# Kernel optimization log

Measured on AMD Instinct MI355X. Metric: run time of the kernel, lower is better.

Reference implementation:

```python
import jax, jax.numpy as jnp
import numpy as np

L, V, C, H, T_MAX, FF = 8, 50257, 1024, 16, 1024, 4096
DH = C // H
EPS = 1e-5


def setup_inputs() -> dict:
    key = jax.random.key(0)
    ks = jax.random.split(key, 16)
    s = 0.02
    inp = {
        "idx": jax.random.randint(ks[0], (2, 1024), 0, V, dtype=jnp.int32),
        "tok_emb": jax.random.normal(ks[1], (V, C), jnp.float32) * s,
        "pos_emb": jax.random.normal(ks[2], (T_MAX, C), jnp.float32) * s,
        "qkv_w": jax.random.normal(ks[3], (L, C, 3 * C), jnp.float32) * s,
        "qkv_b": jnp.zeros((L, 3 * C), jnp.float32),
        "out_w": jax.random.normal(ks[4], (L, C, C), jnp.float32) * s,
        "out_b": jnp.zeros((L, C), jnp.float32),
        "ln1_s": jnp.ones((L, C), jnp.float32),
        "ln1_b": jnp.zeros((L, C), jnp.float32),
        "ln2_s": jnp.ones((L, C), jnp.float32),
        "ln2_b": jnp.zeros((L, C), jnp.float32),
        "ffn_w1": jax.random.normal(ks[5], (L, C, FF), jnp.float32) * s,
        "ffn_b1": jnp.zeros((L, FF), jnp.float32),
        "ffn_w2": jax.random.normal(ks[6], (L, FF, C), jnp.float32) * s,
        "ffn_b2": jnp.zeros((L, C), jnp.float32),
        "lnf_s": jnp.ones((C,), jnp.float32),
        "lnf_b": jnp.zeros((C,), jnp.float32),
    }
    return inp


def _layernorm(x, scale, bias):
    m = jnp.mean(x, axis=-1, keepdims=True)
    v = jnp.mean(jnp.square(x - m), axis=-1, keepdims=True)
    return (x - m) * jax.lax.rsqrt(v + EPS) * scale + bias


def reference(idx, tok_emb, pos_emb, qkv_w, qkv_b, out_w, out_b,
              ln1_s, ln1_b, ln2_s, ln2_b,
              ffn_w1, ffn_b1, ffn_w2, ffn_b2, lnf_s, lnf_b):
    B, T = idx.shape
    x = tok_emb[idx] + pos_emb[:T]          # [B,T,C]
    causal = jnp.tril(jnp.ones((T, T), bool))  # [T,T]
    scale = 1.0 / np.sqrt(DH)

    def block(x, p):
        qw, qb, ow, ob, l1s, l1b, l2s, l2b, w1, b1, w2, b2 = p
        h = _layernorm(x, l1s, l1b)
        qkv = h @ qw + qb                    # [B,T,3C]
        q, k, v = jnp.split(qkv, 3, axis=-1)
        q = q.reshape(B, T, H, DH).transpose(0, 2, 1, 3)  # [B,H,T,Dh]
        k = k.reshape(B, T, H, DH).transpose(0, 2, 1, 3)
        v = v.reshape(B, T, H, DH).transpose(0, 2, 1, 3)
        scores = jnp.einsum('bhqd,bhkd->bhqk', q, k) * scale
        scores = jnp.where(causal, scores, -jnp.inf)
        w = jax.nn.softmax(scores, axis=-1)
        o = jnp.einsum('bhqk,bhkd->bhqd', w, v)
        o = o.transpose(0, 2, 1, 3).reshape(B, T, C)
        x = x + (o @ ow + ob)
        h2 = _layernorm(x, l2s, l2b)
        x = x + (jax.nn.gelu(h2 @ w1 + b1, approximate=False) @ w2 + b2)
        return x, None

    params = (qkv_w, qkv_b, out_w, out_b, ln1_s, ln1_b, ln2_s, ln2_b,
              ffn_w1, ffn_b1, ffn_w2, ffn_b2)
    x, _ = jax.lax.scan(block, x, params)
    x = _layernorm(x, lnf_s, lnf_b)
    logits = x @ tok_emb.T                   # tied head, no bias
    return logits
```

## Files before the change

### kernel.cpp

```cpp
#include <hip/hip_runtime.h>
#include <hip/hip_bf16.h>

#define NL 8
#define NV 50257
#define NC 1024
#define NH 16
#define NT 1024
#define NFF 4096
#define NB 2
#define NM (NB*NT)

typedef __attribute__((ext_vector_type(8))) short bf16x8;
typedef __attribute__((ext_vector_type(4))) float f32x4;

__device__ __forceinline__ unsigned short f2bf(float f) {
    union { float f; unsigned u; } a; a.f = f;
    unsigned r = a.u + 0x7FFFu + ((a.u >> 16) & 1u);
    return (unsigned short)(r >> 16);
}

__device__ __forceinline__ void gload16(const unsigned short* g, unsigned short* l) {
    __builtin_amdgcn_global_load_lds(
        (const __attribute__((address_space(1))) unsigned int*)g,
        (__attribute__((address_space(3))) unsigned int*)l,
        16, 0, 0);
}

template<int VN> __device__ __forceinline__ void vwait() {
    asm volatile("s_waitcnt vmcnt(%0)" :: "n"(VN) : "memory");
}
__device__ __forceinline__ void barrier_mem() {
    asm volatile("" ::: "memory");
    __builtin_amdgcn_s_barrier();
    asm volatile("" ::: "memory");
}

__global__ __launch_bounds__(256) void embed_kernel(
    const int* __restrict__ idx, const float* __restrict__ te,
    const float* __restrict__ pe, float* __restrict__ x) {
    int row = blockIdx.x;
    int t = row & (NT - 1);
    int id = idx[row];
    const float4 a = reinterpret_cast<const float4*>(te + (size_t)id * NC)[threadIdx.x];
    const float4 b = reinterpret_cast<const float4*>(pe + (size_t)t * NC)[threadIdx.x];
    float4 o; o.x = a.x + b.x; o.y = a.y + b.y; o.z = a.z + b.z; o.w = a.w + b.w;
    reinterpret_cast<float4*>(x + (size_t)row * NC)[threadIdx.x] = o;
}

__global__ __launch_bounds__(256) void cvt_bf16_kernel(
    const float* __restrict__ in, unsigned short* __restrict__ out, size_t n4) {
    size_t i = (size_t)blockIdx.x * 256 + threadIdx.x;
    if (i >= n4) return;
    float4 v = reinterpret_cast<const float4*>(in)[i];
    uint2 u;
    u.x = (unsigned)f2bf(v.x) | ((unsigned)f2bf(v.y) << 16);
    u.y = (unsigned)f2bf(v.z) | ((unsigned)f2bf(v.w) << 16);
    reinterpret_cast<uint2*>(out)[i] = u;
}

__global__ __launch_bounds__(256) void wtrans4_kernel(
    const float* __restrict__ s0, const float* __restrict__ s1,
    const float* __restrict__ s2, const float* __restrict__ s3,
    unsigned short* __restrict__ d0, unsigned short* __restrict__ d1,
    unsigned short* __restrict__ d2, unsigned short* __restrict__ d3) {
    __shared__ float tile[32][33];
    int bid = blockIdx.x;
    const float* W; unsigned short* D; int K, N, tn, tk;
    if (bid < 3072)      { W = s0; D = d0; K = 1024; N = 3072; tn = bid % 96;  tk = bid / 96; }
    else if (bid < 4096) { int t = bid - 3072; W = s1; D = d1; K = 1024; N = 1024; tn = t & 31;  tk = t >> 5; }
    else if (bid < 8192) { int t = bid - 4096; W = s2; D = d2; K = 1024; N = 4096; tn = t & 127; tk = t >> 7; }
    else                 { int t = bid - 8192; W = s3; D = d3; K = 4096; N = 1024; tn = t & 31;  tk = t >> 5; }
    int n0 = tn * 32, k0 = tk * 32;
    int tx = threadIdx.x, ty = threadIdx.y;
#pragma unroll
    for (int i = 0; i < 4; ++i)
        tile[ty + i * 8][tx] = W[(size_t)(k0 + ty + i * 8) * N + n0 + tx];
    __syncthreads();
#pragma unroll
    for (int i = 0; i < 4; ++i)
        D[(size_t)(n0 + ty + i * 8) * K + k0 + tx] = f2bf(tile[tx][ty + i * 8]);
}

__global__ __launch_bounds__(256) void ln_kernel(
    const float* __restrict__ x, const float* __restrict__ gam,
    const float* __restrict__ bet, unsigned short* __restrict__ out) {
    __shared__ float red[4];
    int row = blockIdx.x, tid = threadIdx.x;
    const float4 v = reinterpret_cast<const float4*>(x + (size_t)row * NC)[tid];
    float s = v.x + v.y + v.z + v.w;
#pragma unroll
    for (int m = 32; m >= 1; m >>= 1) s += __shfl_xor(s, m, 64);
    if ((tid & 63) == 0) red[tid >> 6] = s;
    __syncthreads();
    float mean = (red[0] + red[1] + red[2] + red[3]) * (1.0f / NC);
    __syncthreads();
    float dx = v.x - mean, dy = v.y - mean, dz = v.z - mean, dw = v.w - mean;
    float q = dx * dx + dy * dy + dz * dz + dw * dw;
#pragma unroll
    for (int m = 32; m >= 1; m >>= 1) q += __shfl_xor(q, m, 64);
    if ((tid & 63) == 0) red[tid >> 6] = q;
    __syncthreads();
    float var = (red[0] + red[1] + red[2] + red[3]) * (1.0f / NC);
    float rstd = rsqrtf(var + 1e-5f);
    int c = tid * 4;
    const float4 g4 = reinterpret_cast<const float4*>(gam)[tid];
    const float4 b4 = reinterpret_cast<const float4*>(bet)[tid];
    uint2 u;
    u.x = (unsigned)f2bf(dx * rstd * g4.x + b4.x) |
          ((unsigned)f2bf(dy * rstd * g4.y + b4.y) << 16);
    u.y = (unsigned)f2bf(dz * rstd * g4.z + b4.z) |
          ((unsigned)f2bf(dw * rstd * g4.w + b4.w) << 16);
    reinterpret_cast<uint2*>(out + (size_t)row * NC + c)[0] = u;
}

template<int ACT, bool BIAS, bool OUTBF16, bool ATOMIC>
__global__ __launch_bounds__(256) void gemm_kernel(
    const unsigned short* __restrict__ A, const unsigned short* __restrict__ Bt,
    const float* __restrict__ bias, void* __restrict__ Cout,
    int N, int K, int ldc, int ksub) {
    __shared__ unsigned short lds[3][2][128 * 32];
    const int tid = threadIdx.x;
    const int lane = tid & 63;
    const int wave = tid >> 6;
    const int wm = wave >> 1, wn = wave & 1;
    const int lr = lane & 15, lg = lane >> 4;
    const int m0 = blockIdx.x * 128, n0 = blockIdx.y * 128;
    const int kbeg = blockIdx.z * ksub;

    const int r0 = tid >> 2;
    const int c0 = (tid & 3) * 8;
    const unsigned short* Ag0 = A + (size_t)(m0 + r0) * K + c0;
    const unsigned short* Ag1 = A + (size_t)(m0 + r0 + 64) * K + c0;
    const unsigned short* Bg0 = Bt + (size_t)(n0 + r0) * K + c0;
    const unsigned short* Bg1 = Bt + (size_t)(n0 + r0 + 64) * K + c0;
    const int dw0 = wave * 512;
    const int dw1 = 2048 + wave * 512;

    const f32x4 zero4 = {0.0f, 0.0f, 0.0f, 0.0f};
    f32x4 acc[4][4];
#pragma unroll
    for (int i = 0; i < 4; ++i)
#pragma unroll
        for (int j = 0; j < 4; ++j) acc[i][j] = zero4;

    auto stage = [&](int buf, int k0) {
        gload16(Ag0 + k0, &lds[buf][0][dw0]);
        gload16(Ag1 + k0, &lds[buf][0][dw1]);
        gload16(Bg0 + k0, &lds[buf][1][dw0]);
        gload16(Bg1 + k0, &lds[buf][1][dw1]);
    };

    const int nt = ksub >> 5;
    stage(0, kbeg);
    stage(1, kbeg + 32);
    vwait<4>();
    barrier_mem();
    int b0 = 0, b1 = 1, b2 = 2;
    for (int t = 0; t < nt; ++t) {
        const bool pf = (t + 2 < nt);
        if (pf) stage(b2, kbeg + (t + 2) * 32);
        bf16x8 af[4], bfr[4];
#pragma unroll
        for (int f = 0; f < 4; ++f) {
            af[f]  = *reinterpret_cast<const bf16x8*>(&lds[b0][0][(wm * 64 + f * 16 + lr) * 32 + lg * 8]);
            bfr[f] = *reinterpret_cast<const bf16x8*>(&lds[b0][1][(wn * 64 + f * 16 + lr) * 32 + lg * 8]);
        }
#pragma unroll
        for (int i = 0; i < 4; ++i)
#pragma unroll
            for (int j = 0; j < 4; ++j)
                acc[i][j] = __builtin_amdgcn_mfma_f32_16x16x32_bf16(af[i], bfr[j], acc[i][j], 0, 0, 0);
        if (t + 1 < nt) {
            if (pf) vwait<4>(); else vwait<0>();
            barrier_mem();
        }
        int tmp = b0; b0 = b1; b1 = b2; b2 = tmp;
    }

#pragma unroll
    for (int i = 0; i < 4; ++i) {
#pragma unroll
        for (int j = 0; j < 4; ++j) {
            int col = n0 + wn * 64 + j * 16 + lr;
            float bv = (BIAS && kbeg == 0) ? bias[col] : 0.0f;
#pragma unroll
            for (int r = 0; r < 4; ++r) {
                int row = m0 + wm * 64 + i * 16 + lg * 4 + r;
                float v = acc[i][j][r] + bv;
                if (ACT == 1) v = 0.5f * v * (1.0f + erff(v * 0.70710678118654752f));
                if (ATOMIC) {
                    atomicAdd(reinterpret_cast<float*>(Cout) + (size_t)row * ldc + col, v);
                } else if (OUTBF16) {
                    reinterpret_cast<unsigned short*>(Cout)[(size_t)row * ldc + col] = f2bf(v);
                } else {
                    reinterpret_cast<float*>(Cout)[(size_t)row * ldc + col] = v;
                }
            }
        }
    }
}

__global__ __launch_bounds__(512, 2) void head_gemm_kernel(
    const unsigned short* __restrict__ A, const unsigned short* __restrict__ Bt,
    float* __restrict__ C, int N, int K) {
    __shared__ unsigned short lds[4][2][8192];
    const int tid = threadIdx.x;
    const int lane = tid & 63, wid = tid >> 6;
    const int wm = wid >> 2, wn = wid & 3;
    const int lr = lane & 15, lg = lane >> 4;

    const int qx = gridDim.x >> 3;
    const int orig = blockIdx.x;
    const int wg = (orig & 7) * qx + (orig >> 3);
    const int m0 = (wg & 7) * 256;
    const int n0 = (wg >> 3) * 256;

    const int o0 = tid, o1 = tid + 512;
    int rA0, kb0, rA1, kb1;
    { int pr = o0 >> 3, s = o0 & 7; int li = (s << 4) ^ ((pr & 7) << 4);
      rA0 = (pr << 1) | (li >> 6); kb0 = li & 63; }
    { int pr = o1 >> 3, s = o1 & 7; int li = (s << 4) ^ ((pr & 7) << 4);
      rA1 = (pr << 1) | (li >> 6); kb1 = li & 63; }
    const char* pA0 = (const char*)A + (size_t)(m0 + rA0) * (2 * K) + kb0;
    const char* pA1 = (const char*)A + (size_t)(m0 + rA1) * (2 * K) + kb1;
    const char* pB0 = (const char*)Bt + (size_t)min(n0 + rA0, N - 1) * (2 * K) + kb0;
    const char* pB1 = (const char*)Bt + (size_t)min(n0 + rA1, N - 1) * (2 * K) + kb1;
    const int dw0 = wid * 512;
    const int dw1 = 4096 + wid * 512;

    const int swz = (((lr & 1) << 6) | (lg << 4)) ^ (((lr >> 1) & 7) << 4);
    const int pbA = (wm * 64 + (lr >> 1)) * 128 + swz;
    const int pbB = (wn * 32 + (lr >> 1)) * 128 + swz;

    auto stage = [&](int slot, int koff) {
        unsigned short* la = &lds[slot][0][0];
        unsigned short* lb = &lds[slot][1][0];
        gload16((const unsigned short*)(pA0 + koff), la + dw0);
        gload16((const unsigned short*)(pA1 + koff), la + dw1);
        gload16((const unsigned short*)(pB0 + koff), lb + dw0);
        gload16((const unsigned short*)(pB1 + koff), lb + dw1);
    };
    auto rdA = [&](int slot, int mf) -> bf16x8 {
        return *reinterpret_cast<const bf16x8*>(
            (const char*)lds + slot * 32768 + pbA + mf * 1024);
    };
    auto rdB = [&](int slot, int nf) -> bf16x8 {
        return *reinterpret_cast<const bf16x8*>(
            (const char*)lds + slot * 32768 + 16384 + pbB + nf * 1024);
    };

    const f32x4 zero4 = {0.0f, 0.0f, 0.0f, 0.0f};
    f32x4 acc[8][4];
#pragma unroll
    for (int i = 0; i < 8; ++i)
#pragma unroll
        for (int j = 0; j < 4; ++j) acc[i][j] = zero4;

#define MFMA_ROW(AF, MI) \
    acc[MI][0] = __builtin_amdgcn_mfma_f32_16x16x32_bf16(AF, bf0, acc[MI][0], 0, 0, 0); \
    acc[MI][1] = __builtin_amdgcn_mfma_f32_16x16x32_bf16(AF, bf1, acc[MI][1], 0, 0, 0); \
    acc[MI][2] = __builtin_amdgcn_mfma_f32_16x16x32_bf16(AF, bf2, acc[MI][2], 0, 0, 0); \
    acc[MI][3] = __builtin_amdgcn_mfma_f32_16x16x32_bf16(AF, bf3, acc[MI][3], 0, 0, 0);

    stage(0, 0);
    stage(1, 64);
    const int nk = K >> 6;
    for (int t = 0; t < nk; ++t) {
        const int cur = (t & 1) << 1;
        const int koff = t << 7;
        const bool pf = (t + 1 < nk);
        vwait<4>();
        barrier_mem();
        if (pf) stage(cur ^ 2, koff + 128);
        bf16x8 bf0 = rdB(cur, 0), bf1 = rdB(cur, 1), bf2 = rdB(cur, 2), bf3 = rdB(cur, 3);
        bf16x8 a0 = rdA(cur, 0), a1 = rdA(cur, 1), a2 = rdA(cur, 2), a3 = rdA(cur, 3);
        __builtin_amdgcn_s_setprio(1);
        MFMA_ROW(a0, 0) MFMA_ROW(a1, 1) MFMA_ROW(a2, 2) MFMA_ROW(a3, 3)
        __builtin_amdgcn_s_setprio(0);
        if (pf) stage((cur ^ 2) | 1, koff + 192);
        a0 = rdA(cur, 4); a1 = rdA(cur, 5); a2 = rdA(cur, 6); a3 = rdA(cur, 7);
        __builtin_amdgcn_s_setprio(1);
        MFMA_ROW(a0, 4) MFMA_ROW(a1, 5) MFMA_ROW(a2, 6) MFMA_ROW(a3, 7)
        __builtin_amdgcn_s_setprio(0);
        if (pf) vwait<8>(); else vwait<0>();
        barrier_mem();
        const int nxt = cur | 1;
        bf0 = rdB(nxt, 0); bf1 = rdB(nxt, 1); bf2 = rdB(nxt, 2); bf3 = rdB(nxt, 3);
        a0 = rdA(nxt, 0); a1 = rdA(nxt, 1); a2 = rdA(nxt, 2); a3 = rdA(nxt, 3);
        __builtin_amdgcn_s_setprio(1);
        MFMA_ROW(a0, 0) MFMA_ROW(a1, 1) MFMA_ROW(a2, 2) MFMA_ROW(a3, 3)
        __builtin_amdgcn_s_setprio(0);
        a0 = rdA(nxt, 4); a1 = rdA(nxt, 5); a2 = rdA(nxt, 6); a3 = rdA(nxt, 7);
        __builtin_amdgcn_s_setprio(1);
        MFMA_ROW(a0, 4) MFMA_ROW(a1, 5) MFMA_ROW(a2, 6) MFMA_ROW(a3, 7)
        __builtin_amdgcn_s_setprio(0);
    }
#undef MFMA_ROW

#pragma unroll
    for (int mf = 0; mf < 8; ++mf)
#pragma unroll
        for (int nf = 0; nf < 4; ++nf) {
            int col = n0 + wn * 64 + nf * 16 + lr;
            if (col < N) {
#pragma unroll
                for (int r = 0; r < 4; ++r) {
                    int row = m0 + wm * 128 + mf * 16 + lg * 4 + r;
                    C[(size_t)row * N + col] = acc[mf][nf][r];
                }
            }
        }
}

__global__ __launch_bounds__(256) void vtrans_kernel(
    const unsigned short* __restrict__ qkv, unsigned short* __restrict__ vt) {
    __shared__ unsigned short tile[32][33];
    int bh = blockIdx.z; int b = bh >> 4, h = bh & 15;
    int t0 = blockIdx.x * 32, d0 = blockIdx.y * 32;
    int tx = threadIdx.x, ty = threadIdx.y;
#pragma unroll
    for (int i = 0; i < 4; ++i)
        tile[ty + i * 8][tx] =
            qkv[(size_t)(b * NT + t0 + ty + i * 8) * 3072 + 2048 + h * 64 + d0 + tx];
    __syncthreads();
#pragma unroll
    for (int i = 0; i < 4; ++i)
        vt[((size_t)(b * NH + h) * 64 + d0 + ty + i * 8) * NT + t0 + tx] = tile[tx][ty + i * 8];
}

__global__ __launch_bounds__(64) void attn_kernel(
    const unsigned short* __restrict__ qkv, const unsigned short* __restrict__ vt,
    unsigned short* __restrict__ o) {
    __shared__ unsigned short Vs[64][72];
    __shared__ unsigned short Ps[32][72];
    const int qt = blockIdx.x;
    const int h  = blockIdx.y;
    const int b  = blockIdx.z;
    const int lane = threadIdx.x;
    const int lr = lane & 15, lg = lane >> 4;

    const unsigned short* qbase = qkv + (size_t)(b * NT + qt * 32) * 3072 + h * 64;
    bf16x8 qf[2][2];
#pragma unroll
    for (int mf = 0; mf < 2; ++mf)
#pragma unroll
        for (int kc = 0; kc < 2; ++kc)
            qf[mf][kc] = *reinterpret_cast<const bf16x8*>(
                qbase + (size_t)(mf * 16 + lr) * 3072 + kc * 32 + lg * 8);

    const f32x4 zero4 = {0.0f, 0.0f, 0.0f, 0.0f};
    f32x4 oacc[2][4];
    float mrow[2][4], lsum[2][4];
#pragma unroll
    for (int mf = 0; mf < 2; ++mf) {
#pragma unroll
        for (int nf = 0; nf < 4; ++nf) oacc[mf][nf] = zero4;
#pragma unroll
        for (int r = 0; r < 4; ++r) { mrow[mf][r] = -INFINITY; lsum[mf][r] = 0.0f; }
    }

    const int qend = qt * 32 + 32;
    const int nkt = (qend + 63) >> 6;
    const unsigned short* kbase = qkv + (size_t)(b * NT) * 3072 + NC + h * 64;
    const unsigned short* vbase = vt + (size_t)((b * NH + h) * 64) * NT;

    for (int kt = 0; kt < nkt; ++kt) {
        __syncthreads();
#pragma unroll
        for (int i = 0; i < 8; ++i) {
            int chunk = lane + i * 64;
            int d = chunk >> 3;
            int kk = (chunk & 7) * 8;
            *reinterpret_cast<bf16x8*>(&Vs[d][kk]) =
                *reinterpret_cast<const bf16x8*>(vbase + (size_t)d * NT + kt * 64 + kk);
        }
        f32x4 s[2][4];
#pragma unroll
        for (int mf = 0; mf < 2; ++mf)
#pragma unroll
            for (int jf = 0; jf < 4; ++jf) s[mf][jf] = zero4;
#pragma unroll
        for (int kc = 0; kc < 2; ++kc) {
            bf16x8 kf[4];
#pragma unroll
            for (int jf = 0; jf < 4; ++jf)
                kf[jf] = *reinterpret_cast<const bf16x8*>(
                    kbase + (size_t)(kt * 64 + jf * 16 + lr) * 3072 + kc * 32 + lg * 8);
#pragma unroll
            for (int mf = 0; mf < 2; ++mf)
#pragma unroll
                for (int jf = 0; jf < 4; ++jf)
                    s[mf][jf] = __builtin_amdgcn_mfma_f32_16x16x32_bf16(
                        qf[mf][kc], kf[jf], s[mf][jf], 0, 0, 0);
        }
        const bool lastt = (kt == nkt - 1);
#pragma unroll
        for (int mf = 0; mf < 2; ++mf) {
#pragma unroll
            for (int r = 0; r < 4; ++r) {
                int rowg = qt * 32 + mf * 16 + lg * 4 + r;
                float tmax = -INFINITY;
#pragma unroll
                for (int jf = 0; jf < 4; ++jf) {
                    float v = s[mf][jf][r] * 0.125f;
                    if (lastt) {
                        int colg = kt * 64 + jf * 16 + lr;
                        if (colg > rowg) v = -INFINITY;
                    }
                    s[mf][jf][r] = v;
                    tmax = fmaxf(tmax, v);
                }
                tmax = fmaxf(tmax, __shfl_xor(tmax, 1, 64));
                tmax = fmaxf(tmax, __shfl_xor(tmax, 2, 64));
                tmax = fmaxf(tmax, __shfl_xor(tmax, 4, 64));
                tmax = fmaxf(tmax, __shfl_xor(tmax, 8, 64));
                float mnew = fmaxf(mrow[mf][r], tmax);
                float corr = __expf(mrow[mf][r] - mnew);
                float ps = 0.0f;
#pragma unroll
                for (int jf = 0; jf < 4; ++jf) {
                    float p = __expf(s[mf][jf][r] - mnew);
                    s[mf][jf][r] = p;
                    ps += p;
                }
                ps += __shfl_xor(ps, 1, 64);
                ps += __shfl_xor(ps, 2, 64);
                ps += __shfl_xor(ps, 4, 64);
                ps += __shfl_xor(ps, 8, 64);
                lsum[mf][r] = lsum[mf][r] * corr + ps;
                mrow[mf][r] = mnew;
#pragma unroll
                for (int nf = 0; nf < 4; ++nf) oacc[mf][nf][r] *= corr;
            }
        }
#pragma unroll
        for (int mf = 0; mf < 2; ++mf)
#pragma unroll
            for (int jf = 0; jf < 4; ++jf)
#pragma unroll
                for (int r = 0; r < 4; ++r)
                    Ps[mf * 16 + lg * 4 + r][jf * 16 + lr] = f2bf(s[mf][jf][r]);
        __syncthreads();
#pragma unroll
        for (int kc = 0; kc < 2; ++kc) {
            bf16x8 pf[2], vf[4];
#pragma unroll
            for (int mf = 0; mf < 2; ++mf)
                pf[mf] = *reinterpret_cast<const bf16x8*>(&Ps[mf * 16 + lr][kc * 32 + lg * 8]);
#pragma unroll
            for (int nf = 0; nf < 4; ++nf)
                vf[nf] = *reinterpret_cast<const bf16x8*>(&Vs[nf * 16 + lr][kc * 32 + lg * 8]);
#pragma unroll
            for (int mf = 0; mf < 2; ++mf)
#pragma unroll
                for (int nf = 0; nf < 4; ++nf)
                    oacc[mf][nf] = __builtin_amdgcn_mfma_f32_16x16x32_bf16(
                        pf[mf], vf[nf], oacc[mf][nf], 0, 0, 0);
        }
    }

    unsigned short* ob = o + (size_t)(b * NT + qt * 32) * NC + h * 64;
#pragma unroll
    for (int mf = 0; mf < 2; ++mf)
#pragma unroll
        for (int nf = 0; nf < 4; ++nf)
#pragma unroll
            for (int r = 0; r < 4; ++r) {
                float v = oacc[mf][nf][r] / lsum[mf][r];
                ob[(size_t)(mf * 16 + lg * 4 + r) * NC + nf * 16 + lr] = f2bf(v);
            }
}

extern "C" void kernel_launch(void* const* d_in, const int* in_sizes, int n_in,
                              void* d_out, int out_size, void* d_ws, size_t ws_size,
                              hipStream_t stream) {
    (void)in_sizes; (void)n_in; (void)out_size; (void)ws_size;
    const int*   idx    = (const int*)  d_in[0];
    const float* tok    = (const float*)d_in[1];
    const float* pos    = (const float*)d_in[2];
    const float* qkv_w  = (const float*)d_in[3];
    const float* qkv_b  = (const float*)d_in[4];
    const float* out_w  = (const float*)d_in[5];
    const float* out_b  = (const float*)d_in[6];
    const float* ln1_s  = (const float*)d_in[7];
    const float* ln1_b  = (const float*)d_in[8];
    const float* ln2_s  = (const float*)d_in[9];
    const float* ln2_b  = (const float*)d_in[10];
    const float* ffn_w1 = (const float*)d_in[11];
    const float* ffn_b1 = (const float*)d_in[12];
    const float* ffn_w2 = (const float*)d_in[13];
    const float* ffn_b2 = (const float*)d_in[14];
    const float* lnf_s  = (const float*)d_in[15];
    const float* lnf_b  = (const float*)d_in[16];

    char* p = (char*)d_ws;
    float* x              = (float*)p;          p += (size_t)NM * NC * 4;
    unsigned short* hbuf  = (unsigned short*)p; p += (size_t)NM * NC * 2;
    unsigned short* qkvb  = (unsigned short*)p; p += (size_t)NM * 3 * NC * 2;
    unsigned short* obuf  = (unsigned short*)p; p += (size_t)NM * NC * 2;
    unsigned short* gbuf  = (unsigned short*)p; p += (size_t)NM * NFF * 2;
    unsigned short* vtb   = (unsigned short*)p; p += (size_t)NB * NH * 64 * NT * 2;
    unsigned short* wq    = (unsigned short*)p; p += (size_t)3 * NC * NC * 2;
    unsigned short* wo    = (unsigned short*)p; p += (size_t)NC * NC * 2;
    unsigned short* w1    = (unsigned short*)p; p += (size_t)NC * NFF * 2;
    unsigned short* w2    = (unsigned short*)p; p += (size_t)NFF * NC * 2;
    unsigned short* temb  = (unsigned short*)p; p += (size_t)NV * NC * 2;

    {
        size_t n4 = (size_t)NV * NC / 4;
        int blocks = (int)((n4 + 255) / 256);
        cvt_bf16_kernel<<<blocks, 256, 0, stream>>>(tok, temb, n4);
    }
    embed_kernel<<<NM, 256, 0, stream>>>(idx, tok, pos, x);

    for (int l = 0; l < NL; ++l) {
        wtrans4_kernel<<<12288, dim3(32, 8), 0, stream>>>(
            qkv_w + (size_t)l * NC * 3 * NC, out_w + (size_t)l * NC * NC,
            ffn_w1 + (size_t)l * NC * NFF, ffn_w2 + (size_t)l * NFF * NC,
            wq, wo, w1, w2);

        ln_kernel<<<NM, 256, 0, stream>>>(x, ln1_s + (size_t)l * NC, ln1_b + (size_t)l * NC, hbuf);
        gemm_kernel<0, true, true, false><<<dim3(16, 24), 256, 0, stream>>>(
            hbuf, wq, qkv_b + (size_t)l * 3 * NC, qkvb, 3 * NC, NC, 3 * NC, NC);
        vtrans_kernel<<<dim3(32, 2, 32), dim3(32, 8), 0, stream>>>(qkvb, vtb);
        attn_kernel<<<dim3(32, 16, 2), 64, 0, stream>>>(qkvb, vtb, obuf);
        gemm_kernel<0, true, false, true><<<dim3(16, 8, 2), 256, 0, stream>>>(
            obuf, wo, out_b + (size_t)l * NC, x, NC, NC, NC, NC / 2);
        ln_kernel<<<NM, 256, 0, stream>>>(x, ln2_s + (size_t)l * NC, ln2_b + (size_t)l * NC, hbuf);
        gemm_kernel<1, true, true, false><<<dim3(16, 32), 256, 0, stream>>>(
            hbuf, w1, ffn_b1 + (size_t)l * NFF, gbuf, NFF, NC, NFF, NC);
        gemm_kernel<0, true, false, true><<<dim3(16, 8, 4), 256, 0, stream>>>(
            gbuf, w2, ffn_b2 + (size_t)l * NC, x, NC, NFF, NC, NFF / 4);
    }
    ln_kernel<<<NM, 256, 0, stream>>>(x, lnf_s, lnf_b, hbuf);
    head_gemm_kernel<<<dim3(8 * 197), 512, 0, stream>>>(hbuf, temb, (float*)d_out, NV, NC);
}
```

Measured before the change: 1.968 ms.

## Shrink LM-head GEMM tile to 128x256 with triple-buffered 32-wide K stages

The vocabulary-projection GEMM now uses 128x256 output tiles instead of 256x256, launching twice as many workgroups. The K pipeline changes from double-buffered 64-wide stages to a three-slot ring of 32-wide stages, with one barrier per step. The aim is to cut LDS and register use per block so more blocks can run per CU, and to simplify the prefetch schedule. In exchange, each tile reuses operands less, there are more barriers per unit of work, and the launch bound of 4 blocks per CU may not fit in LDS.

```diff
diff --git a/kernel.cpp b/kernel.cpp
--- a/kernel.cpp
+++ b/kernel.cpp
@@ -200,10 +200,10 @@
     }
 }
 
-__global__ __launch_bounds__(512, 2) void head_gemm_kernel(
+__global__ __launch_bounds__(512, 4) void head_gemm_kernel(
     const unsigned short* __restrict__ A, const unsigned short* __restrict__ Bt,
     float* __restrict__ C, int N, int K) {
-    __shared__ unsigned short lds[4][2][8192];
+    __shared__ unsigned short lds[3][12288];
     const int tid = threadIdx.x;
     const int lane = tid & 63, wid = tid >> 6;
     const int wm = wid >> 2, wn = wid & 3;
@@ -212,100 +212,102 @@
     const int qx = gridDim.x >> 3;
     const int orig = blockIdx.x;
     const int wg = (orig & 7) * qx + (orig >> 3);
-    const int m0 = (wg & 7) * 256;
-    const int n0 = (wg >> 3) * 256;
-
-    const int o0 = tid, o1 = tid + 512;
-    int rA0, kb0, rA1, kb1;
-    { int pr = o0 >> 3, s = o0 & 7; int li = (s << 4) ^ ((pr & 7) << 4);
-      rA0 = (pr << 1) | (li >> 6); kb0 = li & 63; }
-    { int pr = o1 >> 3, s = o1 & 7; int li = (s << 4) ^ ((pr & 7) << 4);
-      rA1 = (pr << 1) | (li >> 6); kb1 = li & 63; }
-    const char* pA0 = (const char*)A + (size_t)(m0 + rA0) * (2 * K) + kb0;
-    const char* pA1 = (const char*)A + (size_t)(m0 + rA1) * (2 * K) + kb1;
-    const char* pB0 = (const char*)Bt + (size_t)min(n0 + rA0, N - 1) * (2 * K) + kb0;
-    const char* pB1 = (const char*)Bt + (size_t)min(n0 + rA1, N - 1) * (2 * K) + kb1;
-    const int dw0 = wid * 512;
-    const int dw1 = 4096 + wid * 512;
+    const int m0 = (wg & 15) * 128;
+    const int n0 = (wg >> 4) * 256;
+
+    int rA, kA;
+    { int pr = tid >> 3, s = tid & 7; int li = s ^ (pr & 7);
+      rA = 2 * pr + (li >> 2); kA = (li & 3) << 4; }
+    int rB1, kB1;
+    { int o = tid + 512; int pr = o >> 3, s = o & 7; int li = s ^ (pr & 7);
+      rB1 = 2 * pr + (li >> 2); kB1 = (li & 3) << 4; }
+    const char* pAg  = (const char*)A  + (size_t)(m0 + rA) * (2 * K) + kA;
+    const char* pBg0 = (const char*)Bt + (size_t)min(n0 + rA, N - 1) * (2 * K) + kA;
+    const char* pBg1 = (const char*)Bt + (size_t)min(n0 + rB1, N - 1) * (2 * K) + kB1;
+    const int dst = wid * 512;
 
     const int swz = (((lr & 1) << 6) | (lg << 4)) ^ (((lr >> 1) & 7) << 4);
-    const int pbA = (wm * 64 + (lr >> 1)) * 128 + swz;
+    const int pbA = (wm * 32 + (lr >> 1)) * 128 + swz;
     const int pbB = (wn * 32 + (lr >> 1)) * 128 + swz;
 
     auto stage = [&](int slot, int koff) {
-        unsigned short* la = &lds[slot][0][0];
-        unsigned short* lb = &lds[slot][1][0];
-        gload16((const unsigned short*)(pA0 + koff), la + dw0);
-        gload16((const unsigned short*)(pA1 + koff), la + dw1);
-        gload16((const unsigned short*)(pB0 + koff), lb + dw0);
-        gload16((const unsigned short*)(pB1 + koff), lb + dw1);
+        unsigned short* base = &lds[slot][0];
+        gload16((const unsigned short*)(pAg  + koff), base + dst);
+        gload16((const unsigned short*)(pBg0 + koff), base + 4096 + dst);
+        gload16((const unsigned short*)(pBg1 + koff), base + 4096 + dst);
+    };
+    (void)stage;
+
+    const f32x4 zero4 = {0.0f, 0.0f, 0.0f, 0.0f};
+    f32x4 acc[4][4];
+#pragma unroll
+    for (int i = 0; i < 4; ++i)
+#pragma unroll
+        for (int j = 0; j < 4; ++j) acc[i][j] = zero4;
+
+    auto stage3 = [&](int slot, int koff) {
+        unsigned short* base = &lds[slot][0];
+        gload16((const unsigned short*)(pAg  + koff), base + dst);
+        gload16((const unsigned short*)(pBg0 + koff), base + 4096 + dst);
+        gload16((const unsigned short*)(pBg1 + koff), base + 8192 + dst);
     };
     auto rdA = [&](int slot, int mf) -> bf16x8 {
         return *reinterpret_cast<const bf16x8*>(
-            (const char*)lds + slot * 32768 + pbA + mf * 1024);
+            (const char*)&lds[slot][0] + pbA + mf * 1024);
     };
     auto rdB = [&](int slot, int nf) -> bf16x8 {
         return *reinterpret_cast<const bf16x8*>(
-            (const char*)lds + slot * 32768 + 16384 + pbB + nf * 1024);
+            (const char*)&lds[slot][0] + 8192 + pbB + nf * 1024);
     };
 
-    const f32x4 zero4 = {0.0f, 0.0f, 0.0f, 0.0f};
-    f32x4 acc[8][4];
-#pragma unroll
-    for (int i = 0; i < 8; ++i)
-#pragma unroll
-        for (int j = 0; j < 4; ++j) acc[i][j] = zero4;
-
-#define MFMA_ROW(AF, MI) \
-    acc[MI][0] = __builtin_amdgcn_mfma_f32_16x16x32_bf16(AF, bf0, acc[MI][0], 0, 0, 0); \
-    acc[MI][1] = __builtin_amdgcn_mfma_f32_16x16x32_bf16(AF, bf1, acc[MI][1], 0, 0, 0); \
-    acc[MI][2] = __builtin_amdgcn_mfma_f32_16x16x32_bf16(AF, bf2, acc[MI][2], 0, 0, 0); \
-    acc[MI][3] = __builtin_amdgcn_mfma_f32_16x16x32_bf16(AF, bf3, acc[MI][3], 0, 0, 0);
-
-    stage(0, 0);
-    stage(1, 64);
-    const int nk = K >> 6;
-    for (int t = 0; t < nk; ++t) {
-        const int cur = (t & 1) << 1;
-        const int koff = t << 7;
-        const bool pf = (t + 1 < nk);
-        vwait<4>();
-        barrier_mem();
-        if (pf) stage(cur ^ 2, koff + 128);
-        bf16x8 bf0 = rdB(cur, 0), bf1 = rdB(cur, 1), bf2 = rdB(cur, 2), bf3 = rdB(cur, 3);
-        bf16x8 a0 = rdA(cur, 0), a1 = rdA(cur, 1), a2 = rdA(cur, 2), a3 = rdA(cur, 3);
+    const int nt = K >> 5;
+    stage3(0, 0);
+    stage3(1, 64);
+    vwait<3>();
+    barrier_mem();
+    int b0 = 0, b1 = 1, b2 = 2;
+    for (int t = 0; t < nt; ++t) {
+        const bool pf = (t + 2 < nt);
+        if (pf) stage3(b2, (t + 2) * 64);
+        bf16x8 bf0 = rdB(b0, 0), bf1 = rdB(b0, 1), bf2 = rdB(b0, 2), bf3 = rdB(b0, 3);
+        bf16x8 a0 = rdA(b0, 0), a1 = rdA(b0, 1), a2 = rdA(b0, 2), a3 = rdA(b0, 3);
         __builtin_amdgcn_s_setprio(1);
-        MFMA_ROW(a0, 0) MFMA_ROW(a1, 1) MFMA_ROW(a2, 2) MFMA_ROW(a3, 3)
+#pragma unroll
+        for (int dummy = 0; dummy < 1; ++dummy) {
+            acc[0][0] = __builtin_amdgcn_mfma_f32_16x16x32_bf16(a0, bf0, acc[0][0], 0, 0, 0);
+            acc[0][1] = __builtin_amdgcn_mfma_f32_16x16x32_bf16(a0, bf1, acc[0][1], 0, 0, 0);
+            acc[0][2] = __builtin_amdgcn_mfma_f32_16x16x32_bf16(a0, bf2, acc[0][2], 0, 0, 0);
+            acc[0][3] = __builtin_amdgcn_mfma_f32_16x16x32_bf16(a0, bf3, acc[0][3], 0, 0, 0);
+            acc[1][0] = __builtin_amdgcn_mfma_f32_16x16x32_bf16(a1, bf0, acc[1][0], 0, 0, 0);
+            acc[1][1] = __builtin_amdgcn_mfma_f32_16x16x32_bf16(a1, bf1, acc[1][1], 0, 0, 0);
+            acc[1][2] = __builtin_amdgcn_mfma_f32_16x16x32_bf16(a1, bf2, acc[1][2], 0, 0, 0);
+            acc[1][3] = __builtin_amdgcn_mfma_f32_16x16x32_bf16(a1, bf3, acc[1][3], 0, 0, 0);
+            acc[2][0] = __builtin_amdgcn_mfma_f32_16x16x32_bf16(a2, bf0, acc[2][0], 0, 0, 0);
+            acc[2][1] = __builtin_amdgcn_mfma_f32_16x16x32_bf16(a2, bf1, acc[2][1], 0, 0, 0);
+            acc[2][2] = __builtin_amdgcn_mfma_f32_16x16x32_bf16(a2, bf2, acc[2][2], 0, 0, 0);
+            acc[2][3] = __builtin_amdgcn_mfma_f32_16x16x32_bf16(a2, bf3, acc[2][3], 0, 0, 0);
+            acc[3][0] = __builtin_amdgcn_mfma_f32_16x16x32_bf16(a3, bf0, acc[3][0], 0, 0, 0);
+            acc[3][1] = __builtin_amdgcn_mfma_f32_16x16x32_bf16(a3, bf1, acc[3][1], 0, 0, 0);
+            acc[3][2] = __builtin_amdgcn_mfma_f32_16x16x32_bf16(a3, bf2, acc[3][2], 0, 0, 0);
+            acc[3][3] = __builtin_amdgcn_mfma_f32_16x16x32_bf16(a3, bf3, acc[3][3], 0, 0, 0);
+        }
         __builtin_amdgcn_s_setprio(0);
-        if (pf) stage((cur ^ 2) | 1, koff + 192);
-        a0 = rdA(cur, 4); a1 = rdA(cur, 5); a2 = rdA(cur, 6); a3 = rdA(cur, 7);
-        __builtin_amdgcn_s_setprio(1);
-        MFMA_ROW(a0, 4) MFMA_ROW(a1, 5) MFMA_ROW(a2, 6) MFMA_ROW(a3, 7)
-        __builtin_amdgcn_s_setprio(0);
-        if (pf) vwait<8>(); else vwait<0>();
-        barrier_mem();
-        const int nxt = cur | 1;
-        bf0 = rdB(nxt, 0); bf1 = rdB(nxt, 1); bf2 = rdB(nxt, 2); bf3 = rdB(nxt, 3);
-        a0 = rdA(nxt, 0); a1 = rdA(nxt, 1); a2 = rdA(nxt, 2); a3 = rdA(nxt, 3);
-        __builtin_amdgcn_s_setprio(1);
-        MFMA_ROW(a0, 0) MFMA_ROW(a1, 1) MFMA_ROW(a2, 2) MFMA_ROW(a3, 3)
-        __builtin_amdgcn_s_setprio(0);
-        a0 = rdA(nxt, 4); a1 = rdA(nxt, 5); a2 = rdA(nxt, 6); a3 = rdA(nxt, 7);
-        __builtin_amdgcn_s_setprio(1);
-        MFMA_ROW(a0, 4) MFMA_ROW(a1, 5) MFMA_ROW(a2, 6) MFMA_ROW(a3, 7)
-        __builtin_amdgcn_s_setprio(0);
-    }
-#undef MFMA_ROW
-
-#pragma unroll
-    for (int mf = 0; mf < 8; ++mf)
+        if (t + 1 < nt) {
+            if (pf) vwait<3>(); else vwait<0>();
+            barrier_mem();
+        }
+        int tmp = b0; b0 = b1; b1 = b2; b2 = tmp;
+    }
+
+#pragma unroll
+    for (int mf = 0; mf < 4; ++mf)
 #pragma unroll
         for (int nf = 0; nf < 4; ++nf) {
             int col = n0 + wn * 64 + nf * 16 + lr;
             if (col < N) {
 #pragma unroll
                 for (int r = 0; r < 4; ++r) {
-                    int row = m0 + wm * 128 + mf * 16 + lg * 4 + r;
+                    int row = m0 + wm * 64 + mf * 16 + lg * 4 + r;
                     C[(size_t)row * N + col] = acc[mf][nf][r];
                 }
             }
@@ -533,5 +535,5 @@
             gbuf, w2, ffn_b2 + (size_t)l * NC, x, NC, NFF, NC, NFF / 4);
     }
     ln_kernel<<<NM, 256, 0, stream>>>(x, lnf_s, lnf_b, hbuf);
-    head_gemm_kernel<<<dim3(8 * 197), 512, 0, stream>>>(hbuf, temb, (float*)d_out, NV, NC);
-}
+    head_gemm_kernel<<<dim3(16 * 197), 512, 0, stream>>>(hbuf, temb, (float*)d_out, NV, NC);
+}
```

After: 1.948 ms. No clear change (-1.0%).
